# Kernel tuning notes

Measured on AMD Instinct MI355X. Metric: run time of the kernel, lower is better.

## Reference

```python
import jax, jax.numpy as jnp
import numpy as np

EPS = 1e-5
SLOPE = 0.2
K = 20


def _knn(x, k):
    # x: [B, C, N] -> indices of k nearest neighbors [B, N, k] (self included, largest neg sq dist)
    sq = jnp.sum(x * x, axis=1)  # [B, N]
    pd = 2.0 * jnp.einsum('bcn,bcm->bnm', x, x) - sq[:, :, None] - sq[:, None, :]
    return jax.lax.top_k(pd, k)[1]


def _graph_feature(x, k):
    # x: [B, C, N] -> edge features [B, 2C, N, k]
    B, C, N = x.shape
    idx = _knn(x, k)                                   # [B, N, k]
    xt = jnp.transpose(x, (0, 2, 1))                   # [B, N, C]
    nb = xt[jnp.arange(B)[:, None, None], idx]         # [B, N, k, C] gather neighbors
    ctr = jnp.broadcast_to(xt[:, :, None, :], (B, N, k, C))
    f = jnp.concatenate([nb - ctr, ctr], axis=-1)      # [B, N, k, 2C]
    return jnp.transpose(f, (0, 3, 1, 2))              # [B, 2C, N, k]


def _bn_act(y, g, b, m, v):
    # eval-mode batchnorm over channel axis 1 + leaky relu(0.2); y rank 3 or 4
    shp = (1, -1) + (1,) * (y.ndim - 2)
    scale = (g / jnp.sqrt(v + EPS)).reshape(shp)
    shift = (b - m * g / jnp.sqrt(v + EPS)).reshape(shp)
    y = y * scale + shift
    return jnp.where(y >= 0, y, SLOPE * y)


def _edge_block(x, k, W, g, b, m, v):
    f = _graph_feature(x, k)                           # [B, 2C, N, k]
    y = jnp.einsum('oc,bcnk->bonk', W, f)              # 1x1 conv2d, no bias
    y = _bn_act(y, g, b, m, v)
    return jnp.max(y, axis=-1)                         # max over k neighbors -> [B, O, N]


def setup_inputs() -> dict:
    key = jax.random.key(0)
    ks = jax.random.split(key, 8)
    B, N = 16, 2048
    d = {'object_pc': jax.random.normal(ks[0], (B, N, 3), dtype=jnp.float32)}
    dims = [(64, 6), (64, 128), (128, 128), (256, 256), (256, 512)]
    for i, (o, c) in enumerate(dims, start=1):
        d[f'W{i}'] = jax.random.normal(ks[i], (o, c), dtype=jnp.float32) / np.sqrt(c)
        d[f'g{i}'] = jnp.ones((o,), jnp.float32)
        d[f'b{i}'] = jnp.zeros((o,), jnp.float32)
        d[f'm{i}'] = jnp.zeros((o,), jnp.float32)
        d[f'v{i}'] = jnp.ones((o,), jnp.float32)
    return d


def reference(object_pc, W1, g1, b1, m1, v1, W2, g2, b2, m2, v2,
              W3, g3, b3, m3, v3, W4, g4, b4, m4, v4, W5, g5, b5, m5, v5):
    x = jnp.transpose(object_pc, (0, 2, 1))            # [B, 3, N]
    x1 = _edge_block(x, K, W1, g1, b1, m1, v1)         # [B, 64, N]
    x2 = _edge_block(x1, K, W2, g2, b2, m2, v2)        # [B, 64, N]
    x3 = _edge_block(x2, K, W3, g3, b3, m3, v3)        # [B, 128, N]
    x4 = _edge_block(x3, K, W4, g4, b4, m4, v4)        # [B, 256, N]
    cat = jnp.concatenate([x1, x2, x3, x4], axis=1)    # [B, 512, N]
    y = jnp.einsum('oc,bcn->bon', W5, cat)             # 1x1 conv1d
    y = _bn_act(y, g5, b5, m5, v5)
    return jnp.max(y, axis=-1)                         # global max pool -> [B, emb_dim]
```

## Files before the change

### kernel.cpp

```cpp
#include <hip/hip_runtime.h>

#define NPTS 2048
#define KNN_K 20
#define BATCH 16

constexpr float EPSV   = 1e-5f;
constexpr float SLOPEV = 0.2f;

__device__ __forceinline__ float dot4(float4 a, float4 b, float acc) {
  acc = fmaf(a.x, b.x, acc);
  acc = fmaf(a.y, b.y, acc);
  acc = fmaf(a.z, b.z, acc);
  acc = fmaf(a.w, b.w, acc);
  return acc;
}

#define INSERT20(VAL, IDXV)                                              \
  if ((VAL) > topd[KNN_K - 1]) {                                         \
    float d_ = (VAL); int i_ = (IDXV);                                   \
    _Pragma("unroll")                                                    \
    for (int j_ = 0; j_ < KNN_K; ++j_) {                                 \
      bool sw_ = d_ > topd[j_];                                          \
      float td_ = sw_ ? d_ : topd[j_]; float dd_ = sw_ ? topd[j_] : d_;  \
      int   ti_ = sw_ ? i_ : topi[j_]; int  di_ = sw_ ? topi[j_] : i_;   \
      topd[j_] = td_; d_ = dd_; topi[j_] = ti_; i_ = di_;                \
    }                                                                    \
  }

__global__ void pad_kernel(const float* __restrict__ pc, float* __restrict__ X0P) {
  int i = blockIdx.x * 256 + threadIdx.x;
  float4 v;
  v.x = pc[i * 3 + 0]; v.y = pc[i * 3 + 1]; v.z = pc[i * 3 + 2]; v.w = 0.f;
  ((float4*)X0P)[i] = v;
}

template<int C>
__global__ void sq_kernel(const float* __restrict__ XT, float* __restrict__ SQ) {
  int i = blockIdx.x * 256 + threadIdx.x;
  const float4* r4 = (const float4*)(XT + (long)i * C);
  float s = 0.f;
  #pragma unroll
  for (int c = 0; c < C / 4; ++c) { float4 v = r4[c]; s = dot4(v, v, s); }
  SQ[i] = s;
}

template<int C>
__global__ __launch_bounds__(256, 2) void dist_kernel(const float* __restrict__ X,
                                                      const float* __restrict__ SQc,
                                                      float* __restrict__ D) {
  constexpr int KC = (C % 8 == 0) ? 8 : C;
  __shared__ float As[KC][132];
  __shared__ float Bs[KC][132];
  int lin = blockIdx.x;
  int bb = lin >> 8;
  int tile = lin & 255;
  int tn = tile >> 4, tm = tile & 15;
  int t = threadIdx.x;
  int tx = t & 15, ty = t >> 4;
  long base = (long)bb * NPTS;
  const float* Xb = X + base * C;
  int n0 = tn * 128, m0 = tm * 128;

  float acc[8][8];
  #pragma unroll
  for (int i = 0; i < 8; ++i)
    #pragma unroll
    for (int j = 0; j < 8; ++j) acc[i][j] = 0.f;

  for (int k0 = 0; k0 < C; k0 += KC) {
    for (int e = t; e < 32 * KC; e += 256) {
      int row = e / (KC / 4), c4 = e % (KC / 4);
      float4 v = *(const float4*)(Xb + (long)(n0 + row) * C + k0 + c4 * 4);
      As[c4 * 4 + 0][row] = v.x; As[c4 * 4 + 1][row] = v.y;
      As[c4 * 4 + 2][row] = v.z; As[c4 * 4 + 3][row] = v.w;
    }
    for (int e = t; e < 32 * KC; e += 256) {
      int row = e / (KC / 4), c4 = e % (KC / 4);
      float4 v = *(const float4*)(Xb + (long)(m0 + row) * C + k0 + c4 * 4);
      Bs[c4 * 4 + 0][row] = v.x; Bs[c4 * 4 + 1][row] = v.y;
      Bs[c4 * 4 + 2][row] = v.z; Bs[c4 * 4 + 3][row] = v.w;
    }
    __syncthreads();
    #pragma unroll
    for (int k = 0; k < KC; ++k) {
      float4 a0 = *(const float4*)&As[k][ty * 8];
      float4 a1 = *(const float4*)&As[k][ty * 8 + 4];
      float4 b0 = *(const float4*)&Bs[k][tx * 8];
      float4 b1 = *(const float4*)&Bs[k][tx * 8 + 4];
      float av[8] = {a0.x, a0.y, a0.z, a0.w, a1.x, a1.y, a1.z, a1.w};
      float bv[8] = {b0.x, b0.y, b0.z, b0.w, b1.x, b1.y, b1.z, b1.w};
      #pragma unroll
      for (int i = 0; i < 8; ++i)
        #pragma unroll
        for (int j = 0; j < 8; ++j)
          acc[i][j] = fmaf(av[i], bv[j], acc[i][j]);
    }
    __syncthreads();
  }

  float sqn[8], sqm[8];
  #pragma unroll
  for (int i = 0; i < 8; ++i) sqn[i] = SQc[base + n0 + ty * 8 + i];
  #pragma unroll
  for (int j = 0; j < 8; ++j) sqm[j] = SQc[base + m0 + tx * 8 + j];

  #pragma unroll
  for (int i = 0; i < 8; ++i) {
    float* drow = D + (base + n0 + ty * 8 + i) * NPTS + m0 + tx * 8;
    float4 w0, w1;
    w0.x = fmaf(2.f, acc[i][0], -sqn[i]) - sqm[0];
    w0.y = fmaf(2.f, acc[i][1], -sqn[i]) - sqm[1];
    w0.z = fmaf(2.f, acc[i][2], -sqn[i]) - sqm[2];
    w0.w = fmaf(2.f, acc[i][3], -sqn[i]) - sqm[3];
    w1.x = fmaf(2.f, acc[i][4], -sqn[i]) - sqm[4];
    w1.y = fmaf(2.f, acc[i][5], -sqn[i]) - sqm[5];
    w1.z = fmaf(2.f, acc[i][6], -sqn[i]) - sqm[6];
    w1.w = fmaf(2.f, acc[i][7], -sqn[i]) - sqm[7];
    *(float4*)drow = w0;
    *(float4*)(drow + 4) = w1;
  }
}

__global__ __launch_bounds__(256, 2) void select_kernel(const float* __restrict__ D,
                                                        int* __restrict__ IDXc) {
  __shared__ float ld[256][KNN_K];
  __shared__ int   li[256][KNN_K];
  int t = threadIdx.x;
  int rloc = t >> 3, q = t & 7;
  long row = (long)blockIdx.x * 32 + rloc;
  const float4* dr = (const float4*)(D + row * NPTS + q * 256);

  float topd[KNN_K]; int topi[KNN_K];
  #pragma unroll
  for (int j = 0; j < KNN_K; ++j) { topd[j] = -3e38f; topi[j] = 0; }

  int mb = q * 256;
  #pragma unroll 1
  for (int j4 = 0; j4 < 64; j4 += 4) {
    float4 v0 = dr[j4 + 0];
    float4 v1 = dr[j4 + 1];
    float4 v2 = dr[j4 + 2];
    float4 v3 = dr[j4 + 3];
    int m = mb + j4 * 4;
    INSERT20(v0.x, m + 0);
    INSERT20(v0.y, m + 1);
    INSERT20(v0.z, m + 2);
    INSERT20(v0.w, m + 3);
    INSERT20(v1.x, m + 4);
    INSERT20(v1.y, m + 5);
    INSERT20(v1.z, m + 6);
    INSERT20(v1.w, m + 7);
    INSERT20(v2.x, m + 8);
    INSERT20(v2.y, m + 9);
    INSERT20(v2.z, m + 10);
    INSERT20(v2.w, m + 11);
    INSERT20(v3.x, m + 12);
    INSERT20(v3.y, m + 13);
    INSERT20(v3.z, m + 14);
    INSERT20(v3.w, m + 15);
  }

  #pragma unroll
  for (int j = 0; j < KNN_K; ++j) { ld[t][j] = topd[j]; li[t][j] = topi[j]; }
  __syncthreads();

  if (q == 0) {
    int* dst = IDXc + row * KNN_K;
    int ia[8];
    #pragma unroll
    for (int l = 0; l < 8; ++l) ia[l] = 0;
    for (int j = 0; j < KNN_K; ++j) {
      float best = ld[t][ia[0]]; int bl = 0;
      #pragma unroll
      for (int l = 1; l < 8; ++l) {
        float v = ld[t + l][ia[l]];
        if (v > best) { best = v; bl = l; }
      }
      dst[j] = li[t + bl][ia[bl]];
      #pragma unroll
      for (int l = 0; l < 8; ++l) ia[l] += (l == bl) ? 1 : 0;
    }
  }
}

template<int O, int C>
__global__ __launch_bounds__(256, 2) void conv_small(const float* __restrict__ XTin,
                                                     const int* __restrict__ IDX,
                                                     const float* __restrict__ W,
                                                     const float* __restrict__ gg,
                                                     const float* __restrict__ bbias,
                                                     const float* __restrict__ mmean,
                                                     const float* __restrict__ vvar,
                                                     float* __restrict__ XTout) {
  constexpr int G   = 256 / O;
  constexpr int KPG = KNN_K / G;
  __shared__ float cols[KNN_K + 1][C];

  int bid = blockIdx.x;
  int b = bid >> 11, n = bid & 2047;
  int t = threadIdx.x;
  long rowbase = ((long)b << 11);
  const int* idxp = IDX + (long)bid * KNN_K;

  for (int e = t; e < (KNN_K + 1) * C; e += 256) {
    int col = e / C, c = e - col * C;
    int j = (col == 0) ? n : idxp[col - 1];
    cols[col][c] = XTin[(rowbase + j) * C + c];
  }
  __syncthreads();

  int o = t / G, kg = t - o * G;
  const float* wrow = W + o * (2 * C);

  float acc[KPG];
  #pragma unroll
  for (int q = 0; q < KPG; ++q) acc[q] = 0.f;
  float s1 = 0.f, u2 = 0.f;

  #pragma unroll
  for (int c = 0; c < C; ++c) {
    float w1 = wrow[c];
    float w2 = wrow[C + c];
    float xn = cols[0][c];
    s1 = fmaf(w1, xn, s1);
    u2 = fmaf(w2, xn, u2);
    #pragma unroll
    for (int q = 0; q < KPG; ++q) {
      int k = kg * KPG + q;
      acc[q] = fmaf(w1, cols[1 + k][c], acc[q]);
    }
  }

  float sc = gg[o] / sqrtf(vvar[o] + EPSV);
  float sh = bbias[o] - mmean[o] * sc;
  float vmax = -3e38f;
  #pragma unroll
  for (int q = 0; q < KPG; ++q) {
    float z = acc[q] - s1 + u2;
    float y = fmaf(sc, z, sh);
    y = (y >= 0.f) ? y : SLOPEV * y;
    vmax = fmaxf(vmax, y);
  }
  #pragma unroll
  for (int off = 1; off < G; off <<= 1)
    vmax = fmaxf(vmax, __shfl_xor(vmax, off, 64));
  if (kg == 0) XTout[(rowbase + n) * O + o] = vmax;
}

template<int O, int C>
__global__ __launch_bounds__(256, 2) void ad_kernel(const float* __restrict__ X,
                                                    const float* __restrict__ W,
                                                    float* __restrict__ A,
                                                    float* __restrict__ BASE) {
  static_assert(C % 4 == 0 && 256 % O == 0, "ad shape");
  constexpr int G  = 256 / O;
  constexpr int NP = 16 / G;
  constexpr int C4 = C / 4;
  __shared__ float xs[16][C];

  int blk = blockIdx.x;
  long m0 = (long)blk * 16;
  int t = threadIdx.x;

  for (int e = t; e < 16 * C4; e += 256) {
    int pt = e / C4, c4 = e - pt * C4;
    *(float4*)&xs[pt][c4 * 4] = *(const float4*)(X + (m0 + pt) * C + c4 * 4);
  }
  __syncthreads();

  int o = t % O, pg = t / O;
  const float* wrow = W + o * (2 * C);

  float accA[NP], accD[NP];
  #pragma unroll
  for (int q = 0; q < NP; ++q) { accA[q] = 0.f; accD[q] = 0.f; }

  for (int c4 = 0; c4 < C4; ++c4) {
    float4 w1 = *(const float4*)(wrow + c4 * 4);
    float4 w2 = *(const float4*)(wrow + C + c4 * 4);
    #pragma unroll
    for (int q = 0; q < NP; ++q) {
      float4 xv = *(const float4*)&xs[pg * NP + q][c4 * 4];
      accA[q] = dot4(w1, xv, accA[q]);
      accD[q] = dot4(w2, xv, accD[q]);
    }
  }

  #pragma unroll
  for (int q = 0; q < NP; ++q) {
    long m = m0 + pg * NP + q;
    A[m * O + o]    = accA[q];
    BASE[m * O + o] = accD[q] - accA[q];
  }
}

template<int O>
__global__ __launch_bounds__(256, 4) void gather_kernel(const float* __restrict__ A,
                                                        const int* __restrict__ IDX,
                                                        const float* __restrict__ gg,
                                                        const float* __restrict__ bbias,
                                                        const float* __restrict__ mmean,
                                                        const float* __restrict__ vvar,
                                                        float* __restrict__ XTio) {
  constexpr int PPB = 256 / O;
  int t = threadIdx.x;
  int o = t % O, pp = t / O;
  long p = (long)blockIdx.x * PPB + pp;
  int b = (int)(p >> 11);
  long rowbase = ((long)b << 11);
  const int* idxp = IDX + p * KNN_K;

  float base = XTio[p * O + o];
  float sc = gg[o] / sqrtf(vvar[o] + EPSV);
  float sh = bbias[o] - mmean[o] * sc;

  float vmax = -3e38f;
  #pragma unroll
  for (int k = 0; k < KNN_K; ++k) {
    int nb = idxp[k];
    float a = A[(rowbase + nb) * O + o];
    float y = fmaf(sc, a + base, sh);
    y = (y >= 0.f) ? y : SLOPEV * y;
    vmax = fmaxf(vmax, y);
  }
  XTio[p * O + o] = vmax;
}

__global__ __launch_bounds__(256, 2) void final_kernel(const float* __restrict__ X1,
                                                       const float* __restrict__ X2,
                                                       const float* __restrict__ X3,
                                                       const float* __restrict__ X4,
                                                       const float* __restrict__ W5,
                                                       const float* __restrict__ g5,
                                                       const float* __restrict__ b5,
                                                       const float* __restrict__ m5,
                                                       const float* __restrict__ v5,
                                                       float* __restrict__ RED) {
  __shared__ float tile[16][512];
  int bid = blockIdx.x;
  int b = bid >> 7, chunk = bid & 127;
  int n0 = chunk * 16;
  int t = threadIdx.x;

  for (int e = t; e < 16 * 128; e += 256) {
    int nn = e >> 7, c4 = e & 127;
    int c = c4 * 4;
    long row = ((long)b << 11) + n0 + nn;
    float4 v;
    if      (c < 64)  v = *(const float4*)(X1 + row * 64  + c);
    else if (c < 128) v = *(const float4*)(X2 + row * 64  + (c - 64));
    else if (c < 256) v = *(const float4*)(X3 + row * 128 + (c - 128));
    else              v = *(const float4*)(X4 + row * 256 + (c - 256));
    *(float4*)&tile[nn][c] = v;
  }
  __syncthreads();

  int o = t;
  const float* wrow = W5 + o * 512;
  float acc[16];
  #pragma unroll
  for (int q = 0; q < 16; ++q) acc[q] = 0.f;
  for (int c4 = 0; c4 < 128; ++c4) {
    float4 w = *(const float4*)(wrow + c4 * 4);
    #pragma unroll
    for (int q = 0; q < 16; ++q) {
      float4 xv = *(const float4*)&tile[q][c4 * 4];
      acc[q] = dot4(w, xv, acc[q]);
    }
  }
  float sc = g5[o] / sqrtf(v5[o] + EPSV);
  float sh = b5[o] - m5[o] * sc;
  float vmax = -3e38f;
  #pragma unroll
  for (int q = 0; q < 16; ++q) {
    float y = fmaf(sc, acc[q], sh);
    y = (y >= 0.f) ? y : SLOPEV * y;
    vmax = fmaxf(vmax, y);
  }
  RED[((long)b * 256 + o) * 128 + chunk] = vmax;
}

__global__ void reduce_kernel(const float* __restrict__ RED, float* __restrict__ out) {
  int i = blockIdx.x * 256 + threadIdx.x;
  const float* r = RED + (long)i * 128;
  float v = r[0];
  for (int j = 1; j < 128; ++j) v = fmaxf(v, r[j]);
  out[i] = v;
}

extern "C" void kernel_launch(void* const* d_in, const int* in_sizes, int n_in,
                              void* d_out, int out_size, void* d_ws, size_t ws_size,
                              hipStream_t stream) {
  (void)in_sizes; (void)n_in; (void)out_size; (void)ws_size;
  const float* pc = (const float*)d_in[0];
  const float* W1 = (const float*)d_in[1];
  const float* g1 = (const float*)d_in[2];
  const float* b1 = (const float*)d_in[3];
  const float* m1 = (const float*)d_in[4];
  const float* v1 = (const float*)d_in[5];
  const float* W2 = (const float*)d_in[6];
  const float* g2 = (const float*)d_in[7];
  const float* b2 = (const float*)d_in[8];
  const float* m2 = (const float*)d_in[9];
  const float* v2 = (const float*)d_in[10];
  const float* W3 = (const float*)d_in[11];
  const float* g3 = (const float*)d_in[12];
  const float* b3 = (const float*)d_in[13];
  const float* m3 = (const float*)d_in[14];
  const float* v3 = (const float*)d_in[15];
  const float* W4 = (const float*)d_in[16];
  const float* g4 = (const float*)d_in[17];
  const float* b4 = (const float*)d_in[18];
  const float* m4 = (const float*)d_in[19];
  const float* v4 = (const float*)d_in[20];
  const float* W5 = (const float*)d_in[21];
  const float* g5 = (const float*)d_in[22];
  const float* b5 = (const float*)d_in[23];
  const float* m5 = (const float*)d_in[24];
  const float* v5 = (const float*)d_in[25];
  float* out = (float*)d_out;

  float* XT1 = (float*)d_ws;
  float* XT2 = XT1 + 2097152;
  float* XT3 = XT2 + 2097152;
  float* XT4 = XT3 + 4194304;
  float* AD  = XT4 + 8388608;
  float* D   = XT4;
  float* SQ  = AD  + 8388608;
  float* RED = SQ  + 32768;
  int*   IDX = (int*)(RED + 524288);
  float* X0P = (float*)(IDX + 655360);

  const int BN = BATCH * NPTS;
  const long CHB = 4L * NPTS;

  pad_kernel<<<BN / 256, 256, 0, stream>>>(pc, X0P);
  sq_kernel<4><<<BN / 256, 256, 0, stream>>>(X0P, SQ);
  for (int ch = 0; ch < 4; ++ch) {
    dist_kernel<4><<<1024, 256, 0, stream>>>(X0P + ch * CHB * 4, SQ + ch * CHB, D);
    select_kernel<<<256, 256, 0, stream>>>(D, IDX + ch * CHB * KNN_K);
  }
  conv_small<64, 3><<<BN, 256, 0, stream>>>(pc, IDX, W1, g1, b1, m1, v1, XT1);

  sq_kernel<64><<<BN / 256, 256, 0, stream>>>(XT1, SQ);
  for (int ch = 0; ch < 4; ++ch) {
    dist_kernel<64><<<1024, 256, 0, stream>>>(XT1 + ch * CHB * 64, SQ + ch * CHB, D);
    select_kernel<<<256, 256, 0, stream>>>(D, IDX + ch * CHB * KNN_K);
  }
  ad_kernel<64, 64><<<BN / 16, 256, 0, stream>>>(XT1, W2, AD, XT2);
  gather_kernel<64><<<BN / 4, 256, 0, stream>>>(AD, IDX, g2, b2, m2, v2, XT2);

  sq_kernel<64><<<BN / 256, 256, 0, stream>>>(XT2, SQ);
  for (int ch = 0; ch < 4; ++ch) {
    dist_kernel<64><<<1024, 256, 0, stream>>>(XT2 + ch * CHB * 64, SQ + ch * CHB, D);
    select_kernel<<<256, 256, 0, stream>>>(D, IDX + ch * CHB * KNN_K);
  }
  ad_kernel<128, 64><<<BN / 16, 256, 0, stream>>>(XT2, W3, AD, XT3);
  gather_kernel<128><<<BN / 2, 256, 0, stream>>>(AD, IDX, g3, b3, m3, v3, XT3);

  sq_kernel<128><<<BN / 256, 256, 0, stream>>>(XT3, SQ);
  for (int ch = 0; ch < 4; ++ch) {
    dist_kernel<128><<<1024, 256, 0, stream>>>(XT3 + ch * CHB * 128, SQ + ch * CHB, D);
    select_kernel<<<256, 256, 0, stream>>>(D, IDX + ch * CHB * KNN_K);
  }
  ad_kernel<256, 128><<<BN / 16, 256, 0, stream>>>(XT3, W4, AD, XT4);
  gather_kernel<256><<<BN, 256, 0, stream>>>(AD, IDX, g4, b4, m4, v4, XT4);

  final_kernel<<<BATCH * 128, 256, 0, stream>>>(XT1, XT2, XT3, XT4, W5, g5, b5, m5, v5, RED);
  reduce_kernel<<<BATCH, 256, 0, stream>>>(RED, out);
}
```

Measured before the change: 2.630 ms.

## Exploit distance matrix symmetry: compute upper-triangle tiles and write transposes

The pairwise distance kernel now launches only the 136 upper-triangular 128x128 tiles per batch instead of all 256. Each off-diagonal tile writes its result twice, once directly and once transposed through a shared-memory staging buffer, so the GEMM work is roughly halved. The cost is extra shared memory, a serialized transpose loop with 16 barriers per off-diagonal block, and the same total global write traffic, which may limit the benefit if the kernel is store-bound.

```diff
diff --git a/kernel.cpp b/kernel.cpp
--- a/kernel.cpp
+++ b/kernel.cpp
@@ -51,10 +51,13 @@
   constexpr int KC = (C % 8 == 0) ? 8 : C;
   __shared__ float As[KC][132];
   __shared__ float Bs[KC][132];
+  __shared__ float Ts[16][132];
   int lin = blockIdx.x;
-  int bb = lin >> 8;
-  int tile = lin & 255;
-  int tn = tile >> 4, tm = tile & 15;
+  int bb = lin / 136;
+  int tid = lin - bb * 136;
+  int tn = 0, rem = tid;
+  while (rem >= 16 - tn) { rem -= 16 - tn; ++tn; }
+  int tm = tn + rem;
   int t = threadIdx.x;
   int tx = t & 15, ty = t >> 4;
   long base = (long)bb * NPTS;
@@ -105,19 +108,38 @@
   for (int j = 0; j < 8; ++j) sqm[j] = SQc[base + m0 + tx * 8 + j];
 
   #pragma unroll
+  for (int i = 0; i < 8; ++i)
+    #pragma unroll
+    for (int j = 0; j < 8; ++j)
+      acc[i][j] = fmaf(2.f, acc[i][j], -sqn[i]) - sqm[j];
+
+  #pragma unroll
   for (int i = 0; i < 8; ++i) {
     float* drow = D + (base + n0 + ty * 8 + i) * NPTS + m0 + tx * 8;
     float4 w0, w1;
-    w0.x = fmaf(2.f, acc[i][0], -sqn[i]) - sqm[0];
-    w0.y = fmaf(2.f, acc[i][1], -sqn[i]) - sqm[1];
-    w0.z = fmaf(2.f, acc[i][2], -sqn[i]) - sqm[2];
-    w0.w = fmaf(2.f, acc[i][3], -sqn[i]) - sqm[3];
-    w1.x = fmaf(2.f, acc[i][4], -sqn[i]) - sqm[4];
-    w1.y = fmaf(2.f, acc[i][5], -sqn[i]) - sqm[5];
-    w1.z = fmaf(2.f, acc[i][6], -sqn[i]) - sqm[6];
-    w1.w = fmaf(2.f, acc[i][7], -sqn[i]) - sqm[7];
+    w0.x = acc[i][0]; w0.y = acc[i][1]; w0.z = acc[i][2]; w0.w = acc[i][3];
+    w1.x = acc[i][4]; w1.y = acc[i][5]; w1.z = acc[i][6]; w1.w = acc[i][7];
     *(float4*)drow = w0;
     *(float4*)(drow + 4) = w1;
+  }
+
+  if (tn != tm) {
+    for (int s = 0; s < 8; ++s) {
+      if ((tx >> 1) == s) {
+        #pragma unroll
+        for (int j = 0; j < 8; ++j)
+          #pragma unroll
+          for (int i = 0; i < 8; ++i)
+            Ts[(tx & 1) * 8 + j][ty * 8 + i] = acc[i][j];
+      }
+      __syncthreads();
+      for (int e = t; e < 16 * 32; e += 256) {
+        int rr = e >> 5, c4 = e & 31;
+        *(float4*)(D + (base + m0 + s * 16 + rr) * NPTS + n0 + c4 * 4) =
+            *(const float4*)&Ts[rr][c4 * 4];
+      }
+      __syncthreads();
+    }
   }
 }
 
@@ -433,18 +455,19 @@
 
   const int BN = BATCH * NPTS;
   const long CHB = 4L * NPTS;
+  const int DG = 4 * 136;
 
   pad_kernel<<<BN / 256, 256, 0, stream>>>(pc, X0P);
   sq_kernel<4><<<BN / 256, 256, 0, stream>>>(X0P, SQ);
   for (int ch = 0; ch < 4; ++ch) {
-    dist_kernel<4><<<1024, 256, 0, stream>>>(X0P + ch * CHB * 4, SQ + ch * CHB, D);
+    dist_kernel<4><<<DG, 256, 0, stream>>>(X0P + ch * CHB * 4, SQ + ch * CHB, D);
     select_kernel<<<256, 256, 0, stream>>>(D, IDX + ch * CHB * KNN_K);
   }
   conv_small<64, 3><<<BN, 256, 0, stream>>>(pc, IDX, W1, g1, b1, m1, v1, XT1);
 
   sq_kernel<64><<<BN / 256, 256, 0, stream>>>(XT1, SQ);
   for (int ch = 0; ch < 4; ++ch) {
-    dist_kernel<64><<<1024, 256, 0, stream>>>(XT1 + ch * CHB * 64, SQ + ch * CHB, D);
+    dist_kernel<64><<<DG, 256, 0, stream>>>(XT1 + ch * CHB * 64, SQ + ch * CHB, D);
     select_kernel<<<256, 256, 0, stream>>>(D, IDX + ch * CHB * KNN_K);
   }
   ad_kernel<64, 64><<<BN / 16, 256, 0, stream>>>(XT1, W2, AD, XT2);
@@ -452,7 +475,7 @@
 
   sq_kernel<64><<<BN / 256, 256, 0, stream>>>(XT2, SQ);
   for (int ch = 0; ch < 4; ++ch) {
-    dist_kernel<64><<<1024, 256, 0, stream>>>(XT2 + ch * CHB * 64, SQ + ch * CHB, D);
+    dist_kernel<64><<<DG, 256, 0, stream>>>(XT2 + ch * CHB * 64, SQ + ch * CHB, D);
     select_kernel<<<256, 256, 0, stream>>>(D, IDX + ch * CHB * KNN_K);
   }
   ad_kernel<128, 64><<<BN / 16, 256, 0, stream>>>(XT2, W3, AD, XT3);
@@ -460,7 +483,7 @@
 
   sq_kernel<128><<<BN / 256, 256, 0, stream>>>(XT3, SQ);
   for (int ch = 0; ch < 4; ++ch) {
-    dist_kernel<128><<<1024, 256, 0, stream>>>(XT3 + ch * CHB * 128, SQ + ch * CHB, D);
+    dist_kernel<128><<<DG, 256, 0, stream>>>(XT3 + ch * CHB * 128, SQ + ch * CHB, D);
     select_kernel<<<256, 256, 0, stream>>>(D, IDX + ch * CHB * KNN_K);
   }
   ad_kernel<256, 128><<<BN / 16, 256, 0, stream>>>(XT3, W4, AD, XT4);
```

Measured after the change: 2.501 ms. 1.05x faster.
